# Kernel optimization log

Measured on AMD Instinct MI355X. Metric: run time of the kernel, lower is better.

## Reference

```python
import jax, jax.numpy as jnp
import numpy as np

N = 50000      # nodes
DEG = 16       # avg degree (random edges)
D = 128        # input_dim
H = 128        # hidden_dim
EPS = 1e-12


def setup_inputs() -> dict:
    key = jax.random.key(0)
    kx, ks, kd, kw1, kw2 = jax.random.split(key, 5)
    x = jax.random.normal(kx, (N, D), dtype=jnp.float32)
    src = jax.random.randint(ks, (N * DEG,), 0, N)
    dst = jax.random.randint(kd, (N * DEG,), 0, N)
    loops = jnp.arange(N)  # self-loops (AGNNConv default) -> every node has >=1 in-edge
    edge_index = jnp.stack([jnp.concatenate([src, loops]),
                            jnp.concatenate([dst, loops])]).astype(jnp.int64)
    W1 = jax.random.normal(kw1, (D, H), dtype=jnp.float32) / np.float32(np.sqrt(D))
    b1 = jnp.zeros((H,), dtype=jnp.float32)
    W2 = jax.random.normal(kw2, (H, H), dtype=jnp.float32) / np.float32(np.sqrt(H))
    b2 = jnp.zeros((H,), dtype=jnp.float32)
    beta1 = jnp.ones((), dtype=jnp.float32)
    beta2 = jnp.ones((), dtype=jnp.float32)
    return {"x": x, "edge_index": edge_index, "W1": W1, "b1": b1,
            "beta1": beta1, "W2": W2, "b2": b2, "beta2": beta2}


def _agnn_conv(x, edge_index, W, b, beta):
    n = x.shape[0]
    h = x @ W + b                                   # [N, H] linear projection
    # l2-normalize for cosine similarity
    hn = h * jax.lax.rsqrt(jnp.sum(h * h, axis=-1, keepdims=True) + EPS)
    src, dst = edge_index[0], edge_index[1]
    score = beta * jnp.sum(hn[src] * hn[dst], axis=-1)   # [E] beta * cos(h_i, h_j)
    # segment softmax over incoming edges of each destination node
    m = jax.ops.segment_max(score, dst, num_segments=n)
    e = jnp.exp(score - m[dst])
    denom = jax.ops.segment_sum(e, dst, num_segments=n)
    alpha = e / denom[dst]                               # [E]
    # weighted aggregation of source features
    return jax.ops.segment_sum(alpha[:, None] * h[src], dst, num_segments=n)


def reference(x, edge_index, W1, b1, beta1, W2, b2, beta2):
    h = jax.nn.relu(_agnn_conv(x, edge_index, W1, b1, beta1))
    # dropout (p=0.1) is identity in eval mode
    return jax.nn.relu(_agnn_conv(h, edge_index, W2, b2, beta2))
```

## Files before the change

kernel.cpp:

```cpp
#include <hip/hip_runtime.h>
#include <hip/hip_bf16.h>
#include <hip/hip_fp16.h>


#define FDIM 128
#define SCAN_CHUNK 2048
#define CSTRIDE 32

template <typename TIN>
__device__ __forceinline__ void gemm_body(
    const TIN* __restrict__ X, const float* __restrict__ Wg,
    const float* __restrict__ bias, __half* __restrict__ H16,
    float* __restrict__ rnorm, int N, int bid) {
  __shared__ float xt[128][72];
  int tid = threadIdx.x;
  int wv = tid >> 6, lane = tid & 63;
  int rowgrp = lane >> 5;
  int colgrp = lane & 31;
  int rbase = wv * 16 + rowgrp * 8;
  float4 bj = ((const float4*)bias)[colgrp];
  int r0 = bid * 64;

  for (int idx = tid; idx < 64 * 128; idx += 256) {
    int rr = idx >> 7, cc = idx & 127;
    int r = r0 + rr; if (r >= N) r = N - 1;
    xt[cc][rr] = (float)X[(size_t)r * 128 + cc];
  }
  __syncthreads();

  float4 a[8];
  #pragma unroll
  for (int rr = 0; rr < 8; ++rr) a[rr] = bj;

  #pragma unroll 4
  for (int k = 0; k < 128; ++k) {
    float4 w = *(const float4*)(Wg + k * 128 + 4 * colgrp);
    float4 xv0 = *(const float4*)&xt[k][rbase];
    float4 xv1 = *(const float4*)&xt[k][rbase + 4];
    a[0].x += xv0.x*w.x; a[0].y += xv0.x*w.y; a[0].z += xv0.x*w.z; a[0].w += xv0.x*w.w;
    a[1].x += xv0.y*w.x; a[1].y += xv0.y*w.y; a[1].z += xv0.y*w.z; a[1].w += xv0.y*w.w;
    a[2].x += xv0.z*w.x; a[2].y += xv0.z*w.y; a[2].z += xv0.z*w.z; a[2].w += xv0.z*w.w;
    a[3].x += xv0.w*w.x; a[3].y += xv0.w*w.y; a[3].z += xv0.w*w.z; a[3].w += xv0.w*w.w;
    a[4].x += xv1.x*w.x; a[4].y += xv1.x*w.y; a[4].z += xv1.x*w.z; a[4].w += xv1.x*w.w;
    a[5].x += xv1.y*w.x; a[5].y += xv1.y*w.y; a[5].z += xv1.y*w.z; a[5].w += xv1.y*w.w;
    a[6].x += xv1.z*w.x; a[6].y += xv1.z*w.y; a[6].z += xv1.z*w.z; a[6].w += xv1.z*w.w;
    a[7].x += xv1.w*w.x; a[7].y += xv1.w*w.y; a[7].z += xv1.w*w.z; a[7].w += xv1.w*w.w;
  }

  #pragma unroll
  for (int rr = 0; rr < 8; ++rr) {
    float4 aa = a[rr];
    float s = aa.x*aa.x + aa.y*aa.y + aa.z*aa.z + aa.w*aa.w;
    #pragma unroll
    for (int m = 16; m; m >>= 1) s += __shfl_xor(s, m);
    int r = r0 + rbase + rr;
    if (r < N) {
      __half2 lo = __floats2half2_rn(aa.x, aa.y);
      __half2 hi = __floats2half2_rn(aa.z, aa.w);
      __half2* dst = (__half2*)(H16 + (size_t)r * 128 + 4 * colgrp);
      dst[0] = lo; dst[1] = hi;
      if (colgrp == 0) rnorm[r] = rsqrtf(s + 1e-12f);
    }
  }
}

__device__ __forceinline__ void convert_body(
    const void* __restrict__ ei, int E,
    int* __restrict__ src32, int* __restrict__ dst32,
    int* __restrict__ rank, int* __restrict__ counts, int cbid) {
  const int* eii = (const int*)ei;
  int lane = threadIdx.x & 63;
  int ok = (lane < 32) ? (eii[2 * lane + 1] == 0) : 1;
  bool is64 = (__ballot(ok) == ~0ull);

  int e = cbid * 256 + threadIdx.x;
  if (e >= E) return;
  int s, d;
  if (is64) {
    const long long* p = (const long long*)ei;
    s = (int)p[e]; d = (int)p[E + e];
  } else {
    s = eii[e]; d = eii[E + e];
  }
  src32[e] = s; dst32[e] = d;
  rank[e] = atomicAdd(&counts[d * CSTRIDE], 1);
}

__global__ __launch_bounds__(256) void gemm1_convert_kernel(
    const float* __restrict__ X, const float* __restrict__ Wg,
    const float* __restrict__ bias, __half* __restrict__ H16,
    float* __restrict__ rnorm, int N, int GB,
    const void* __restrict__ ei, int E,
    int* __restrict__ src32, int* __restrict__ dst32,
    int* __restrict__ rank, int* __restrict__ counts) {
  if ((int)blockIdx.x < GB)
    gemm_body<float>(X, Wg, bias, H16, rnorm, N, blockIdx.x);
  else
    convert_body(ei, E, src32, dst32, rank, counts, blockIdx.x - GB);
}

__global__ __launch_bounds__(256) void gemm_norm_h_kernel(
    const __half* __restrict__ X, const float* __restrict__ Wg,
    const float* __restrict__ bias, __half* __restrict__ H16,
    float* __restrict__ rnorm, int N) {
  gemm_body<__half>(X, Wg, bias, H16, rnorm, N, blockIdx.x);
}

__global__ __launch_bounds__(256) void scan_a_kernel(
    const int* __restrict__ counts, int* __restrict__ bsum, int N) {
  __shared__ int ws[4];
  int tid = threadIdx.x;
  int i0 = blockIdx.x * SCAN_CHUNK + tid * 8;
  int s = 0;
  #pragma unroll
  for (int j = 0; j < 8; ++j)
    if (i0 + j < N) s += counts[(size_t)(i0 + j) * CSTRIDE];
  #pragma unroll
  for (int m = 32; m; m >>= 1) s += __shfl_xor(s, m);
  int lane = tid & 63, wv = tid >> 6;
  if (lane == 0) ws[wv] = s;
  __syncthreads();
  if (tid == 0) bsum[blockIdx.x] = ws[0] + ws[1] + ws[2] + ws[3];
}

__global__ __launch_bounds__(256) void scan_c_kernel(
    const int* __restrict__ counts, const int* __restrict__ bsum,
    int* __restrict__ offsets, int N, int E) {
  __shared__ int wsum[4];
  int tid = threadIdx.x, lane = tid & 63, wv = tid >> 6;

  int bse = 0;
  for (int j = lane; j < (int)blockIdx.x; j += 64) bse += bsum[j];
  #pragma unroll
  for (int m = 32; m; m >>= 1) bse += __shfl_xor(bse, m);

  int i0 = blockIdx.x * SCAN_CHUNK + tid * 8;
  int v[8];
  #pragma unroll
  for (int j = 0; j < 8; ++j)
    v[j] = (i0 + j < N) ? counts[(size_t)(i0 + j) * CSTRIDE] : 0;
  int pre[8], t = 0;
  #pragma unroll
  for (int j = 0; j < 8; ++j) { pre[j] = t; t += v[j]; }
  int x = t;
  #pragma unroll
  for (int off = 1; off < 64; off <<= 1) {
    int u = __shfl_up(x, off);
    if (lane >= off) x += u;
  }
  if (lane == 63) wsum[wv] = x;
  __syncthreads();
  int waveoff = 0;
  #pragma unroll
  for (int w = 0; w < 4; ++w) if (w < wv) waveoff += wsum[w];
  int ebase = bse + waveoff + (x - t);
  #pragma unroll
  for (int j = 0; j < 8; ++j) {
    int i = i0 + j;
    if (i < N) offsets[i] = ebase + pre[j];
  }
  if (blockIdx.x == 0 && tid == 0) offsets[N] = E;
}

__global__ __launch_bounds__(256) void scatter_kernel(
    const int* __restrict__ src32, const int* __restrict__ dst32,
    const int* __restrict__ rank, const int* __restrict__ offsets, int E,
    int* __restrict__ csr_src) {
  int e = blockIdx.x * 256 + threadIdx.x;
  if (e >= E) return;
  csr_src[offsets[dst32[e]] + rank[e]] = src32[e];
}

template <bool OUT_HALF>
__global__ __launch_bounds__(256) void agg_kernel(
    const __half* __restrict__ H16, const float* __restrict__ rnorm,
    const float* __restrict__ beta_p, const int* __restrict__ offsets,
    const int* __restrict__ csr_src, void* __restrict__ Yp, int N) {
  int wid = (blockIdx.x * 256 + threadIdx.x) >> 6;
  int lane = threadIdx.x & 63;
  if (wid >= N) return;
  int g = lane >> 4;
  int l = lane & 15;
  const float4* H4 = (const float4*)H16;

  float4 hdv = H4[(size_t)wid * 16 + l];
  const __half2* hdp = (const __half2*)&hdv;
  float2 d0 = __half22float2(hdp[0]);
  float2 d1 = __half22float2(hdp[1]);
  float2 d2 = __half22float2(hdp[2]);
  float2 d3 = __half22float2(hdp[3]);
  float rdb = rnorm[wid] * beta_p[0];

  int e0 = offsets[wid], e1 = offsets[wid + 1];
  float denom = 0.f;
  float acc[8] = {0.f,0.f,0.f,0.f,0.f,0.f,0.f,0.f};

  int e = e0 + g;
  bool valid = e < e1;
  int s = valid ? csr_src[e] : wid;
  float4 hv = H4[(size_t)s * 16 + l];
  float rs = rnorm[s];

  for (int eb = e0; eb < e1; eb += 4) {
    int en = e + 4;
    bool vn = en < e1;
    int sn = vn ? csr_src[en] : wid;
    float4 hvn = H4[(size_t)sn * 16 + l];
    float rsn = rnorm[sn];

    const __half2* hp = (const __half2*)&hv;
    float2 q0 = __half22float2(hp[0]);
    float2 q1 = __half22float2(hp[1]);
    float2 q2 = __half22float2(hp[2]);
    float2 q3 = __half22float2(hp[3]);
    float p = q0.x*d0.x + q0.y*d0.y + q1.x*d1.x + q1.y*d1.y
            + q2.x*d2.x + q2.y*d2.y + q3.x*d3.x + q3.y*d3.y;
    p += __shfl_xor(p, 1);
    p += __shfl_xor(p, 2);
    p += __shfl_xor(p, 4);
    p += __shfl_xor(p, 8);
    float w = valid ? __expf(p * rdb * rs) : 0.f;
    denom += w;
    acc[0] += w*q0.x; acc[1] += w*q0.y; acc[2] += w*q1.x; acc[3] += w*q1.y;
    acc[4] += w*q2.x; acc[5] += w*q2.y; acc[6] += w*q3.x; acc[7] += w*q3.y;

    e = en; valid = vn; s = sn; hv = hvn; rs = rsn;
  }

  #pragma unroll
  for (int m = 16; m <= 32; m <<= 1) {
    denom += __shfl_xor(denom, m);
    #pragma unroll
    for (int j = 0; j < 8; ++j) acc[j] += __shfl_xor(acc[j], m);
  }
  if (g == 0) {
    float inv = 1.0f / denom;
    float o[8];
    #pragma unroll
    for (int j = 0; j < 8; ++j) o[j] = fmaxf(acc[j] * inv, 0.f);
    if constexpr (OUT_HALF) {
      float4 pack;
      __half2* hp2 = (__half2*)&pack;
      hp2[0] = __floats2half2_rn(o[0], o[1]);
      hp2[1] = __floats2half2_rn(o[2], o[3]);
      hp2[2] = __floats2half2_rn(o[4], o[5]);
      hp2[3] = __floats2half2_rn(o[6], o[7]);
      ((float4*)Yp)[(size_t)wid * 16 + l] = pack;
    } else {
      float4 o0 = {o[0], o[1], o[2], o[3]};
      float4 o1 = {o[4], o[5], o[6], o[7]};
      ((float4*)Yp)[(size_t)wid * 32 + 2 * l] = o0;
      ((float4*)Yp)[(size_t)wid * 32 + 2 * l + 1] = o1;
    }
  }
}

extern "C" void kernel_launch(void* const* d_in, const int* in_sizes, int n_in,
                              void* d_out, int out_size, void* d_ws, size_t ws_size,
                              hipStream_t stream) {
  const float* x     = (const float*)d_in[0];
  const void*  ei    = d_in[1];
  const float* W1    = (const float*)d_in[2];
  const float* b1    = (const float*)d_in[3];
  const float* beta1 = (const float*)d_in[4];
  const float* W2    = (const float*)d_in[5];
  const float* b2    = (const float*)d_in[6];
  const float* beta2 = (const float*)d_in[7];

  int N = in_sizes[0] / FDIM;
  int E = in_sizes[1] / 2;

  char* p = (char*)d_ws;
  auto alloc = [&](size_t bytes) {
    char* r = p; p += (bytes + 255) & ~size_t(255); return r;
  };
  int*    counts  = (int*)alloc(sizeof(int) * (size_t)N * CSTRIDE);
  int*    offsets = (int*)alloc(sizeof(int) * (N + 1));
  int*    bsum    = (int*)alloc(sizeof(int) * 256);
  int*    src32   = (int*)alloc(sizeof(int) * E);
  int*    dst32   = (int*)alloc(sizeof(int) * E);
  int*    rank    = (int*)alloc(sizeof(int) * E);
  int*    csr     = (int*)alloc(sizeof(int) * E);
  __half* h16     = (__half*)alloc(sizeof(__half) * (size_t)N * FDIM);
  float*  rn      = (float*)alloc(sizeof(float) * N);
  __half* y1h     = (__half*)alloc(sizeof(__half) * (size_t)N * FDIM);

  hipMemsetAsync(counts, 0, sizeof(int) * (size_t)N * CSTRIDE, stream);

  int cb = (E + 255) / 256;
  int gb = (N + 63) / 64;
  int nb = (N + SCAN_CHUNK - 1) / SCAN_CHUNK;
  int ab = (N + 3) / 4;

  gemm1_convert_kernel<<<gb + cb, 256, 0, stream>>>(
      x, W1, b1, h16, rn, N, gb, ei, E, src32, dst32, rank, counts);
  scan_a_kernel<<<nb, 256, 0, stream>>>(counts, bsum, N);
  scan_c_kernel<<<nb, 256, 0, stream>>>(counts, bsum, offsets, N, E);
  scatter_kernel<<<cb, 256, 0, stream>>>(src32, dst32, rank, offsets, E, csr);

  agg_kernel<true><<<ab, 256, 0, stream>>>(h16, rn, beta1, offsets, csr, y1h, N);
  gemm_norm_h_kernel<<<gb, 256, 0, stream>>>(y1h, W2, b2, h16, rn, N);
  agg_kernel<false><<<ab, 256, 0, stream>>>(h16, rn, beta2, offsets, csr, d_out, N);
}
```

Measured before the change: 256.6 us.

## Split fused gemm/convert launch and deepen agg gather prefetch to two stages

Undoes the fusion of the first GEMM with the edge-conversion/count kernel, launching them as separate kernels with the GEMM moved after CSR construction. In the aggregation kernel, the software prefetch of neighbor rows is deepened from one iteration ahead to two, so more gather loads are in flight to hide memory latency. The deeper prefetch costs extra registers (another float4 plus index state per lane), and un-fusing adds a launch and removes overlap between GEMM and atomic counting.

```diff
diff --git a/kernel.cpp b/kernel.cpp
--- a/kernel.cpp
+++ b/kernel.cpp
@@ -7,11 +7,98 @@
 #define SCAN_CHUNK 2048
 #define CSTRIDE 32
 
+__global__ __launch_bounds__(256) void convert_count_kernel(
+    const void* __restrict__ ei, int E,
+    int* __restrict__ src32, int* __restrict__ dst32,
+    int* __restrict__ rank, int* __restrict__ counts) {
+  const int* eii = (const int*)ei;
+  int lane = threadIdx.x & 63;
+  int ok = (lane < 32) ? (eii[2 * lane + 1] == 0) : 1;
+  bool is64 = (__ballot(ok) == ~0ull);
+
+  int e = blockIdx.x * 256 + threadIdx.x;
+  if (e >= E) return;
+  int s, d;
+  if (is64) {
+    const long long* p = (const long long*)ei;
+    s = (int)p[e]; d = (int)p[E + e];
+  } else {
+    s = eii[e]; d = eii[E + e];
+  }
+  src32[e] = s; dst32[e] = d;
+  rank[e] = atomicAdd(&counts[d * CSTRIDE], 1);
+}
+
+__global__ __launch_bounds__(256) void scan_a_kernel(
+    const int* __restrict__ counts, int* __restrict__ bsum, int N) {
+  __shared__ int ws[4];
+  int tid = threadIdx.x;
+  int i0 = blockIdx.x * SCAN_CHUNK + tid * 8;
+  int s = 0;
+  #pragma unroll
+  for (int j = 0; j < 8; ++j)
+    if (i0 + j < N) s += counts[(size_t)(i0 + j) * CSTRIDE];
+  #pragma unroll
+  for (int m = 32; m; m >>= 1) s += __shfl_xor(s, m);
+  int lane = tid & 63, wv = tid >> 6;
+  if (lane == 0) ws[wv] = s;
+  __syncthreads();
+  if (tid == 0) bsum[blockIdx.x] = ws[0] + ws[1] + ws[2] + ws[3];
+}
+
+__global__ __launch_bounds__(256) void scan_c_kernel(
+    const int* __restrict__ counts, const int* __restrict__ bsum,
+    int* __restrict__ offsets, int N, int E) {
+  __shared__ int wsum[4];
+  int tid = threadIdx.x, lane = tid & 63, wv = tid >> 6;
+
+  int bse = 0;
+  for (int j = lane; j < (int)blockIdx.x; j += 64) bse += bsum[j];
+  #pragma unroll
+  for (int m = 32; m; m >>= 1) bse += __shfl_xor(bse, m);
+
+  int i0 = blockIdx.x * SCAN_CHUNK + tid * 8;
+  int v[8];
+  #pragma unroll
+  for (int j = 0; j < 8; ++j)
+    v[j] = (i0 + j < N) ? counts[(size_t)(i0 + j) * CSTRIDE] : 0;
+  int pre[8], t = 0;
+  #pragma unroll
+  for (int j = 0; j < 8; ++j) { pre[j] = t; t += v[j]; }
+  int x = t;
+  #pragma unroll
+  for (int off = 1; off < 64; off <<= 1) {
+    int u = __shfl_up(x, off);
+    if (lane >= off) x += u;
+  }
+  if (lane == 63) wsum[wv] = x;
+  __syncthreads();
+  int waveoff = 0;
+  #pragma unroll
+  for (int w = 0; w < 4; ++w) if (w < wv) waveoff += wsum[w];
+  int ebase = bse + waveoff + (x - t);
+  #pragma unroll
+  for (int j = 0; j < 8; ++j) {
+    int i = i0 + j;
+    if (i < N) offsets[i] = ebase + pre[j];
+  }
+  if (blockIdx.x == 0 && tid == 0) offsets[N] = E;
+}
+
+__global__ __launch_bounds__(256) void scatter_kernel(
+    const int* __restrict__ src32, const int* __restrict__ dst32,
+    const int* __restrict__ rank, const int* __restrict__ offsets, int E,
+    int* __restrict__ csr_src) {
+  int e = blockIdx.x * 256 + threadIdx.x;
+  if (e >= E) return;
+  csr_src[offsets[dst32[e]] + rank[e]] = src32[e];
+}
+
 template <typename TIN>
-__device__ __forceinline__ void gemm_body(
+__global__ __launch_bounds__(256) void gemm_norm_kernel(
     const TIN* __restrict__ X, const float* __restrict__ Wg,
     const float* __restrict__ bias, __half* __restrict__ H16,
-    float* __restrict__ rnorm, int N, int bid) {
+    float* __restrict__ rnorm, int N) {
   __shared__ float xt[128][72];
   int tid = threadIdx.x;
   int wv = tid >> 6, lane = tid & 63;
@@ -19,7 +106,7 @@
   int colgrp = lane & 31;
   int rbase = wv * 16 + rowgrp * 8;
   float4 bj = ((const float4*)bias)[colgrp];
-  int r0 = bid * 64;
+  int r0 = blockIdx.x * 64;
 
   for (int idx = tid; idx < 64 * 128; idx += 256) {
     int rr = idx >> 7, cc = idx & 127;
@@ -64,113 +151,6 @@
   }
 }
 
-__device__ __forceinline__ void convert_body(
-    const void* __restrict__ ei, int E,
-    int* __restrict__ src32, int* __restrict__ dst32,
-    int* __restrict__ rank, int* __restrict__ counts, int cbid) {
-  const int* eii = (const int*)ei;
-  int lane = threadIdx.x & 63;
-  int ok = (lane < 32) ? (eii[2 * lane + 1] == 0) : 1;
-  bool is64 = (__ballot(ok) == ~0ull);
-
-  int e = cbid * 256 + threadIdx.x;
-  if (e >= E) return;
-  int s, d;
-  if (is64) {
-    const long long* p = (const long long*)ei;
-    s = (int)p[e]; d = (int)p[E + e];
-  } else {
-    s = eii[e]; d = eii[E + e];
-  }
-  src32[e] = s; dst32[e] = d;
-  rank[e] = atomicAdd(&counts[d * CSTRIDE], 1);
-}
-
-__global__ __launch_bounds__(256) void gemm1_convert_kernel(
-    const float* __restrict__ X, const float* __restrict__ Wg,
-    const float* __restrict__ bias, __half* __restrict__ H16,
-    float* __restrict__ rnorm, int N, int GB,
-    const void* __restrict__ ei, int E,
-    int* __restrict__ src32, int* __restrict__ dst32,
-    int* __restrict__ rank, int* __restrict__ counts) {
-  if ((int)blockIdx.x < GB)
-    gemm_body<float>(X, Wg, bias, H16, rnorm, N, blockIdx.x);
-  else
-    convert_body(ei, E, src32, dst32, rank, counts, blockIdx.x - GB);
-}
-
-__global__ __launch_bounds__(256) void gemm_norm_h_kernel(
-    const __half* __restrict__ X, const float* __restrict__ Wg,
-    const float* __restrict__ bias, __half* __restrict__ H16,
-    float* __restrict__ rnorm, int N) {
-  gemm_body<__half>(X, Wg, bias, H16, rnorm, N, blockIdx.x);
-}
-
-__global__ __launch_bounds__(256) void scan_a_kernel(
-    const int* __restrict__ counts, int* __restrict__ bsum, int N) {
-  __shared__ int ws[4];
-  int tid = threadIdx.x;
-  int i0 = blockIdx.x * SCAN_CHUNK + tid * 8;
-  int s = 0;
-  #pragma unroll
-  for (int j = 0; j < 8; ++j)
-    if (i0 + j < N) s += counts[(size_t)(i0 + j) * CSTRIDE];
-  #pragma unroll
-  for (int m = 32; m; m >>= 1) s += __shfl_xor(s, m);
-  int lane = tid & 63, wv = tid >> 6;
-  if (lane == 0) ws[wv] = s;
-  __syncthreads();
-  if (tid == 0) bsum[blockIdx.x] = ws[0] + ws[1] + ws[2] + ws[3];
-}
-
-__global__ __launch_bounds__(256) void scan_c_kernel(
-    const int* __restrict__ counts, const int* __restrict__ bsum,
-    int* __restrict__ offsets, int N, int E) {
-  __shared__ int wsum[4];
-  int tid = threadIdx.x, lane = tid & 63, wv = tid >> 6;
-
-  int bse = 0;
-  for (int j = lane; j < (int)blockIdx.x; j += 64) bse += bsum[j];
-  #pragma unroll
-  for (int m = 32; m; m >>= 1) bse += __shfl_xor(bse, m);
-
-  int i0 = blockIdx.x * SCAN_CHUNK + tid * 8;
-  int v[8];
-  #pragma unroll
-  for (int j = 0; j < 8; ++j)
-    v[j] = (i0 + j < N) ? counts[(size_t)(i0 + j) * CSTRIDE] : 0;
-  int pre[8], t = 0;
-  #pragma unroll
-  for (int j = 0; j < 8; ++j) { pre[j] = t; t += v[j]; }
-  int x = t;
-  #pragma unroll
-  for (int off = 1; off < 64; off <<= 1) {
-    int u = __shfl_up(x, off);
-    if (lane >= off) x += u;
-  }
-  if (lane == 63) wsum[wv] = x;
-  __syncthreads();
-  int waveoff = 0;
-  #pragma unroll
-  for (int w = 0; w < 4; ++w) if (w < wv) waveoff += wsum[w];
-  int ebase = bse + waveoff + (x - t);
-  #pragma unroll
-  for (int j = 0; j < 8; ++j) {
-    int i = i0 + j;
-    if (i < N) offsets[i] = ebase + pre[j];
-  }
-  if (blockIdx.x == 0 && tid == 0) offsets[N] = E;
-}
-
-__global__ __launch_bounds__(256) void scatter_kernel(
-    const int* __restrict__ src32, const int* __restrict__ dst32,
-    const int* __restrict__ rank, const int* __restrict__ offsets, int E,
-    int* __restrict__ csr_src) {
-  int e = blockIdx.x * 256 + threadIdx.x;
-  if (e >= E) return;
-  csr_src[offsets[dst32[e]] + rank[e]] = src32[e];
-}
-
 template <bool OUT_HALF>
 __global__ __launch_bounds__(256) void agg_kernel(
     const __half* __restrict__ H16, const float* __restrict__ rnorm,
@@ -195,20 +175,26 @@
   float denom = 0.f;
   float acc[8] = {0.f,0.f,0.f,0.f,0.f,0.f,0.f,0.f};
 
-  int e = e0 + g;
-  bool valid = e < e1;
-  int s = valid ? csr_src[e] : wid;
-  float4 hv = H4[(size_t)s * 16 + l];
-  float rs = rnorm[s];
+  int eA = e0 + g;
+  bool vA = eA < e1;
+  int sA = vA ? csr_src[eA] : wid;
+  float4 hA = H4[(size_t)sA * 16 + l];
+  float rA = rnorm[sA];
+
+  int eB = eA + 4;
+  bool vB = eB < e1;
+  int sB = vB ? csr_src[eB] : wid;
+  float4 hB = H4[(size_t)sB * 16 + l];
+  float rB = rnorm[sB];
 
   for (int eb = e0; eb < e1; eb += 4) {
-    int en = e + 4;
-    bool vn = en < e1;
-    int sn = vn ? csr_src[en] : wid;
-    float4 hvn = H4[(size_t)sn * 16 + l];
-    float rsn = rnorm[sn];
-
-    const __half2* hp = (const __half2*)&hv;
+    int eC = eb + 8 + g;
+    bool vC = eC < e1;
+    int sC = vC ? csr_src[eC] : wid;
+    float4 hC = H4[(size_t)sC * 16 + l];
+    float rC = rnorm[sC];
+
+    const __half2* hp = (const __half2*)&hA;
     float2 q0 = __half22float2(hp[0]);
     float2 q1 = __half22float2(hp[1]);
     float2 q2 = __half22float2(hp[2]);
@@ -219,12 +205,13 @@
     p += __shfl_xor(p, 2);
     p += __shfl_xor(p, 4);
     p += __shfl_xor(p, 8);
-    float w = valid ? __expf(p * rdb * rs) : 0.f;
+    float w = vA ? __expf(p * rdb * rA) : 0.f;
     denom += w;
     acc[0] += w*q0.x; acc[1] += w*q0.y; acc[2] += w*q1.x; acc[3] += w*q1.y;
     acc[4] += w*q2.x; acc[5] += w*q2.y; acc[6] += w*q3.x; acc[7] += w*q3.y;
 
-    e = en; valid = vn; s = sn; hv = hvn; rs = rsn;
+    vA = vB; hA = hB; rA = rB;
+    vB = vC; hB = hC; rB = rC;
   }
 
   #pragma unroll
@@ -292,13 +279,13 @@
   int nb = (N + SCAN_CHUNK - 1) / SCAN_CHUNK;
   int ab = (N + 3) / 4;
 
-  gemm1_convert_kernel<<<gb + cb, 256, 0, stream>>>(
-      x, W1, b1, h16, rn, N, gb, ei, E, src32, dst32, rank, counts);
+  convert_count_kernel<<<cb, 256, 0, stream>>>(ei, E, src32, dst32, rank, counts);
   scan_a_kernel<<<nb, 256, 0, stream>>>(counts, bsum, N);
   scan_c_kernel<<<nb, 256, 0, stream>>>(counts, bsum, offsets, N, E);
   scatter_kernel<<<cb, 256, 0, stream>>>(src32, dst32, rank, offsets, E, csr);
 
+  gemm_norm_kernel<float><<<gb, 256, 0, stream>>>(x, W1, b1, h16, rn, N);
   agg_kernel<true><<<ab, 256, 0, stream>>>(h16, rn, beta1, offsets, csr, y1h, N);
-  gemm_norm_h_kernel<<<gb, 256, 0, stream>>>(y1h, W2, b2, h16, rn, N);
+  gemm_norm_kernel<__half><<<gb, 256, 0, stream>>>(y1h, W2, b2, h16, rn, N);
   agg_kernel<false><<<ab, 256, 0, stream>>>(h16, rn, beta2, offsets, csr, d_out, N);
 }
```

New measurement: 276.0 us. +7.6%, slower.
